# Performance work log

Hardware: AMD Instinct MI355X
Metric: run time of the kernel (lower is better)

## Reference

```python
import jax, jax.numpy as jnp
import numpy as np

EPS_NORM = 1e-6
EPS_LN = 1e-5


def setup_inputs() -> dict:
    key = jax.random.key(0)
    ks = jax.random.split(key, 6)
    b, m, d = 8, 1024, 768
    n, p = 64, 16
    h = 2 * d
    x = jax.random.normal(ks[0], (b, m, d), dtype=jnp.float32)
    phi = jax.random.normal(ks[1], (n, p, d), dtype=jnp.float32)
    # per-expert LayerNorm affine params
    ln_g = jnp.ones((n, d), dtype=jnp.float32)
    ln_b = jnp.zeros((n, d), dtype=jnp.float32)
    # per-expert MLP weights (torch Linear default init ~ U(-1/sqrt(fan_in), ...); use scaled normal)
    w1 = jax.random.normal(ks[2], (n, d, h), dtype=jnp.float32) * (1.0 / np.sqrt(d))
    b1 = jax.random.normal(ks[3], (n, h), dtype=jnp.float32) * 0.01
    w2 = jax.random.normal(ks[4], (n, h, d), dtype=jnp.float32) * (1.0 / np.sqrt(h))
    b2 = jax.random.normal(ks[5], (n, d), dtype=jnp.float32) * 0.01
    return {"x": x, "phi": phi, "ln_g": ln_g, "ln_b": ln_b,
            "w1": w1, "b1": b1, "w2": w2, "b2": b2}


def _layernorm(x, g, b):
    mu = jnp.mean(x, axis=-1, keepdims=True)
    var = jnp.mean(jnp.square(x - mu), axis=-1, keepdims=True)
    return (x - mu) * jax.lax.rsqrt(var + EPS_LN) * g + b


def reference(x, phi, ln_g, ln_b, w1, b1, w2, b2):
    # normalize phi over axis=0 (expert axis), as in the torch __init__
    phi_n = phi * jax.lax.rsqrt(jnp.sum(jnp.square(phi), axis=0, keepdims=True) + EPS_NORM)
    bsz, m, d = x.shape
    n, p, _ = phi_n.shape
    # routing logits: [b, m, n, p]
    logits = jnp.einsum('bmd,npd->bmnp', x, phi_n)
    # dispatch: softmax over tokens m
    D = jax.nn.softmax(logits, axis=1)
    # combine: softmax over flattened slots (n*p)
    C = jax.nn.softmax(logits.reshape(bsz, m, n * p), axis=-1)
    # input slots: [b, n, p, d]
    Xs = jnp.einsum('bmd,bmnp->bnpd', x, D)
    # batched per-expert MLP: LN -> Linear -> GELU -> Linear
    hdn = _layernorm(Xs, ln_g[:, None, :], ln_b[:, None, :])
    hdn = jnp.einsum('bnpd,ndh->bnph', hdn, w1) + b1[:, None, :]
    hdn = jax.nn.gelu(hdn, approximate=False)
    Ys = jnp.einsum('bnph,nhd->bnpd', hdn, w2) + b2[:, None, :]
    # combine: [b, m, d]
    Ys = Ys.reshape(bsz, n * p, d)
    Y = jnp.einsum('bsd,bms->bmd', Ys, C)
    return Y
```

## Files before the change

kernel.cpp:

```cpp
#include <hip/hip_runtime.h>
#include <math.h>

#define B 8
#define M 1024
#define D 768
#define NEXP 64
#define P 16
#define H 1536
#define S 1024
#define EPS_NORM 1e-6f
#define EPS_LN   1e-5f

typedef unsigned short u16;
typedef __attribute__((ext_vector_type(8))) short bf16x8;
typedef __attribute__((ext_vector_type(4))) float f32x4;

__device__ __forceinline__ u16 f2bf(float f) {
    union { float f; unsigned u; } v; v.f = f;
    unsigned r = v.u + 0x7FFFu + ((v.u >> 16) & 1u);
    return (u16)(r >> 16);
}

__device__ __forceinline__ float gelu_exact(float x) {
    return 0.5f * x * (1.0f + erff(x * 0.70710678118654752440f));
}

#define GLL16(g, l) __builtin_amdgcn_global_load_lds( \
    (const __attribute__((address_space(1))) void*)(g), \
    (__attribute__((address_space(3))) void*)(l), 16, 0, 0)

__device__ __forceinline__ void mfma_core_128(const u16* __restrict__ Ag,
                                              const u16* __restrict__ Bg,
                                              int K, u16* As, u16* Bs,
                                              f32x4 (&acc)[4][4]) {
    const int t    = threadIdx.x;
    const int lane = t & 63;
    const int wave = t >> 6;
    const int wr   = (wave >> 1) << 6;
    const int wc   = (wave & 1) << 6;
    const int quad = lane >> 4;
    const int l16  = lane & 15;
    const u16* ga0 = Ag + (size_t)(t >> 2) * K + (t & 3) * 8;
    const u16* ga1 = ga0 + (size_t)64 * K;
    const u16* gb0 = Bg + (size_t)(t >> 2) * K + (t & 3) * 8;
    const u16* gb1 = gb0 + (size_t)64 * K;
    u16* la0 = As + t * 8;
    u16* lb0 = Bs + t * 8;
    const u16* arp = As + (wr + l16) * 32 + quad * 8;
    const u16* brp = Bs + (wc + l16) * 32 + quad * 8;
    GLL16(ga0, la0);
    GLL16(ga1, la0 + 2048);
    GLL16(gb0, lb0);
    GLL16(gb1, lb0 + 2048);
    int cur = 0;
    for (int k0 = 0; k0 < K; k0 += 32) {
        __syncthreads();
        const int nxt = cur ^ 1;
        if (k0 + 32 < K) {
            GLL16(ga0 + k0 + 32, la0 + nxt * 4096);
            GLL16(ga1 + k0 + 32, la0 + nxt * 4096 + 2048);
            GLL16(gb0 + k0 + 32, lb0 + nxt * 4096);
            GLL16(gb1 + k0 + 32, lb0 + nxt * 4096 + 2048);
        }
        const u16* ar = arp + cur * 4096;
        const u16* br = brp + cur * 4096;
        bf16x8 af[4], bfr[4];
#pragma unroll
        for (int i = 0; i < 4; ++i) af[i]  = *(const bf16x8*)(ar + i * 512);
#pragma unroll
        for (int j = 0; j < 4; ++j) bfr[j] = *(const bf16x8*)(br + j * 512);
#pragma unroll
        for (int i = 0; i < 4; ++i)
#pragma unroll
            for (int j = 0; j < 4; ++j)
                acc[i][j] = __builtin_amdgcn_mfma_f32_16x16x32_bf16(af[i], bfr[j], acc[i][j], 0, 0, 0);
        cur = nxt;
    }
}

__device__ __forceinline__ void mfma_core_bf32(const u16* __restrict__ Ag, int K,
                                               const float* __restrict__ Bg, int ldb,
                                               u16* As, u16* Bs,
                                               f32x4 (&acc)[4][4]) {
    const int t    = threadIdx.x;
    const int lane = t & 63;
    const int wave = t >> 6;
    const int wr   = (wave >> 1) << 6;
    const int wc   = (wave & 1) << 6;
    const int quad = lane >> 4;
    const int l16  = lane & 15;
    const u16* ga0 = Ag + (size_t)(t >> 2) * K + (t & 3) * 8;
    const u16* ga1 = ga0 + (size_t)64 * K;
    u16* la0 = As + t * 8;
    const int bcol = t & 127;
    const int kq   = (t >> 7) << 4;
    const float* bg0 = Bg + (size_t)kq * ldb + bcol;
    u16* lb = Bs + bcol * 40 + kq;
    const u16* arp = As + (wr + l16) * 32 + quad * 8;
    const u16* brp = Bs + (wc + l16) * 40 + quad * 8;
    GLL16(ga0, la0);
    GLL16(ga1, la0 + 2048);
    {
        float f[16];
#pragma unroll
        for (int i = 0; i < 16; ++i) f[i] = bg0[(size_t)i * ldb];
#pragma unroll
        for (int i = 0; i < 4; ++i) {
            ushort4 o;
            o.x = f2bf(f[i*4 + 0]); o.y = f2bf(f[i*4 + 1]);
            o.z = f2bf(f[i*4 + 2]); o.w = f2bf(f[i*4 + 3]);
            *(ushort4*)(lb + i * 4) = o;
        }
    }
    int cur = 0;
    for (int k0 = 0; k0 < K; k0 += 32) {
        __syncthreads();
        const int nxt = cur ^ 1;
        const bool pf = (k0 + 32 < K);
        float f[16];
        if (pf) {
            GLL16(ga0 + k0 + 32, la0 + nxt * 4096);
            GLL16(ga1 + k0 + 32, la0 + nxt * 4096 + 2048);
            const float* bg = bg0 + (size_t)(k0 + 32) * ldb;
#pragma unroll
            for (int i = 0; i < 16; ++i) f[i] = bg[(size_t)i * ldb];
        }
        const u16* ar = arp + cur * 4096;
        const u16* br = brp + cur * 5120;
        bf16x8 af[4], bfr[4];
#pragma unroll
        for (int i = 0; i < 4; ++i) af[i]  = *(const bf16x8*)(ar + i * 512);
#pragma unroll
        for (int j = 0; j < 4; ++j) bfr[j] = *(const bf16x8*)(br + j * 640);
#pragma unroll
        for (int i = 0; i < 4; ++i)
#pragma unroll
            for (int j = 0; j < 4; ++j)
                acc[i][j] = __builtin_amdgcn_mfma_f32_16x16x32_bf16(af[i], bfr[j], acc[i][j], 0, 0, 0);
        if (pf) {
            u16* lbn = lb + nxt * 5120;
#pragma unroll
            for (int i = 0; i < 4; ++i) {
                ushort4 o;
                o.x = f2bf(f[i*4 + 0]); o.y = f2bf(f[i*4 + 1]);
                o.z = f2bf(f[i*4 + 2]); o.w = f2bf(f[i*4 + 3]);
                *(ushort4*)(lbn + i * 4) = o;
            }
        }
        cur = nxt;
    }
}

#define EPI_VARS \
    const int t = threadIdx.x; const int lane = t & 63; const int wave = t >> 6; \
    const int wr = (wave >> 1) << 6; const int wc = (wave & 1) << 6; \
    const int quad = lane >> 4; const int l16 = lane & 15; (void)t;

#define ACC_INIT \
    f32x4 acc[4][4]; \
    _Pragma("unroll") for (int i = 0; i < 4; ++i) \
    _Pragma("unroll") for (int j = 0; j < 4; ++j) acc[i][j] = (f32x4){0.f, 0.f, 0.f, 0.f};

__global__ __launch_bounds__(256) void prep_fused_kernel(const float* __restrict__ x,
                                                         const float* __restrict__ phi,
                                                         u16* __restrict__ xb,
                                                         u16* __restrict__ xT,
                                                         u16* __restrict__ phinb) {
    if (blockIdx.z == 8) {
        int bid = blockIdx.y * 12 + blockIdx.x;
        if (bid >= 48) return;
        int pos = bid * 256 + threadIdx.x;
        float ss = 0.f;
#pragma unroll 4
        for (int nn = 0; nn < NEXP; ++nn) {
            float v = phi[nn * (P*D) + pos];
            ss += v * v;
        }
        float r = rsqrtf(ss + EPS_NORM);
#pragma unroll 4
        for (int nn = 0; nn < NEXP; ++nn)
            phinb[nn * (P*D) + pos] = f2bf(phi[nn * (P*D) + pos] * r);
        return;
    }
    __shared__ float tile[64][65];
    int b = blockIdx.z;
    int m0 = blockIdx.y * 64, d0 = blockIdx.x * 64;
    int tt = threadIdx.x;
    int rr = tt >> 4, c4 = (tt & 15) * 4;
#pragma unroll
    for (int i = 0; i < 4; ++i) {
        int m = m0 + rr + i * 16;
        float4 v = *(const float4*)(x + ((size_t)b * M + m) * D + d0 + c4);
        tile[rr + i*16][c4 + 0] = v.x;
        tile[rr + i*16][c4 + 1] = v.y;
        tile[rr + i*16][c4 + 2] = v.z;
        tile[rr + i*16][c4 + 3] = v.w;
        ushort4 o;
        o.x = f2bf(v.x); o.y = f2bf(v.y); o.z = f2bf(v.z); o.w = f2bf(v.w);
        *(ushort4*)(xb + ((size_t)b * M + m) * D + d0 + c4) = o;
    }
    __syncthreads();
    int cr = tt >> 4, r4 = (tt & 15) * 4;
#pragma unroll
    for (int i = 0; i < 4; ++i) {
        int crow = cr + i * 16;
        ushort4 o;
        o.x = f2bf(tile[r4 + 0][crow]);
        o.y = f2bf(tile[r4 + 1][crow]);
        o.z = f2bf(tile[r4 + 2][crow]);
        o.w = f2bf(tile[r4 + 3][crow]);
        *(ushort4*)(xT + ((size_t)b * D + d0 + crow) * M + m0 + r4) = o;
    }
}


__global__ __launch_bounds__(256) void gemm_logits_mfma(const u16* __restrict__ xb,
                                                        const u16* __restrict__ phinb,
                                                        float* __restrict__ logits) {
    __shared__ __align__(16) u16 As[8192], Bs[8192];
    ACC_INIT;
    const int row0 = blockIdx.y * 128, col0 = blockIdx.x * 128;
    mfma_core_128(xb + (size_t)row0 * D, phinb + (size_t)col0 * D, D, As, Bs, acc);
    EPI_VARS;
#pragma unroll
    for (int i = 0; i < 4; ++i)
#pragma unroll
        for (int j = 0; j < 4; ++j) {
            int col = col0 + wc + j*16 + l16;
#pragma unroll
            for (int r = 0; r < 4; ++r) {
                int row = row0 + wr + i*16 + quad*4 + r;
                logits[(size_t)row * S + col] = acc[i][j][r];
            }
        }
}

__global__ __launch_bounds__(256) void gemm_dispatch_mfma(const u16* __restrict__ DT,
                                                          const u16* __restrict__ xT,
                                                          float* __restrict__ Xs) {
    __shared__ __align__(16) u16 As[8192], Bs[8192];
    ACC_INIT;
    const int b = blockIdx.z;
    const int row0 = blockIdx.y * 128, col0 = blockIdx.x * 128;
    mfma_core_128(DT + ((size_t)b * S + row0) * M,
                  xT + ((size_t)b * D + col0) * M, M, As, Bs, acc);
    EPI_VARS;
#pragma unroll
    for (int i = 0; i < 4; ++i)
#pragma unroll
        for (int j = 0; j < 4; ++j) {
            int col = col0 + wc + j*16 + l16;
#pragma unroll
            for (int r = 0; r < 4; ++r) {
                int row = row0 + wr + i*16 + quad*4 + r;
                Xs[((size_t)b * S + row) * D + col] = acc[i][j][r];
            }
        }
}

__global__ __launch_bounds__(256) void gemm_mlp1_mfma(const u16* __restrict__ hdnE,
                                                      const float* __restrict__ w1,
                                                      const float* __restrict__ b1,
                                                      u16* __restrict__ h1) {
    __shared__ __align__(16) u16 As[8192], Bs[10240];
    ACC_INIT;
    const int n = blockIdx.z;
    const int col0 = blockIdx.x * 128;
    mfma_core_bf32(hdnE + (size_t)n * 128 * D, D,
                   w1 + (size_t)n * D * H + col0, H, As, Bs, acc);
    EPI_VARS;
#pragma unroll
    for (int i = 0; i < 4; ++i)
#pragma unroll
        for (int j = 0; j < 4; ++j) {
            int h = col0 + wc + j*16 + l16;
            float bias = b1[n * H + h];
#pragma unroll
            for (int r = 0; r < 4; ++r) {
                int row = wr + i*16 + quad*4 + r;
                h1[((size_t)n * 128 + row) * H + h] = f2bf(gelu_exact(acc[i][j][r] + bias));
            }
        }
}

__global__ __launch_bounds__(256) void gemm_mlp2_mfma(const u16* __restrict__ h1,
                                                      const float* __restrict__ w2,
                                                      const float* __restrict__ b2,
                                                      u16* __restrict__ YsT) {
    __shared__ __align__(16) u16 As[8192], Bs[10240];
    ACC_INIT;
    const int n = blockIdx.z;
    const int col0 = blockIdx.x * 128;
    mfma_core_bf32(h1 + (size_t)n * 128 * H, H,
                   w2 + (size_t)n * H * D + col0, D, As, Bs, acc);
    EPI_VARS;
#pragma unroll
    for (int i = 0; i < 4; ++i)
#pragma unroll
        for (int j = 0; j < 4; ++j) {
            int d = col0 + wc + j*16 + l16;
            float bias = b2[n * D + d];
            int bb = ((wr + i*16) >> 4);
            int p0 = quad * 4;
            ushort4 o;
            o.x = f2bf(acc[i][j][0] + bias);
            o.y = f2bf(acc[i][j][1] + bias);
            o.z = f2bf(acc[i][j][2] + bias);
            o.w = f2bf(acc[i][j][3] + bias);
            *(ushort4*)(YsT + ((size_t)bb * D + d) * S + n * P + p0) = o;
        }
}

__global__ __launch_bounds__(256) void gemm_combine_mfma(const u16* __restrict__ Cb,
                                                         const u16* __restrict__ YsT,
                                                         float* __restrict__ out) {
    __shared__ __align__(16) u16 As[8192], Bs[8192];
    ACC_INIT;
    const int b = blockIdx.z;
    const int row0 = blockIdx.y * 128, col0 = blockIdx.x * 128;
    mfma_core_128(Cb + ((size_t)b * M + row0) * S,
                  YsT + ((size_t)b * D + col0) * S, S, As, Bs, acc);
    EPI_VARS;
#pragma unroll
    for (int i = 0; i < 4; ++i)
#pragma unroll
        for (int j = 0; j < 4; ++j) {
            int col = col0 + wc + j*16 + l16;
#pragma unroll
            for (int r = 0; r < 4; ++r) {
                int row = row0 + wr + i*16 + quad*4 + r;
                out[((size_t)b * M + row) * D + col] = acc[i][j][r];
            }
        }
}

__global__ __launch_bounds__(256) void smcol_kernel(const float* __restrict__ logits,
                                                    u16* __restrict__ Cb,
                                                    float* __restrict__ pm,
                                                    float* __restrict__ pl) {
    __shared__ float lm[3][1024], ll[3][1024];
    const int c2   = blockIdx.x;
    const int b    = c2 >> 5;
    const int mgrp = c2 & 31;
    const int t    = threadIdx.x;
    const int w    = t >> 6;
    const int lane = t & 63;
    float cm[16], cl[16];
#pragma unroll
    for (int i = 0; i < 16; ++i) { cm[i] = -INFINITY; cl[i] = 0.f; }
    const size_t rbase = (size_t)(b * 1024 + mgrp * 32 + w * 8) * 1024;
    const float* Lb = logits + rbase;
    u16* Cbb = Cb + rbase;
    for (int r = 0; r < 8; ++r) {
        const float* row = Lb + (size_t)r * 1024;
        float4 v[4];
#pragma unroll
        for (int q = 0; q < 4; ++q)
            v[q] = *(const float4*)(row + q * 256 + lane * 4);
        float mx = -INFINITY;
#pragma unroll
        for (int q = 0; q < 4; ++q)
            mx = fmaxf(mx, fmaxf(fmaxf(v[q].x, v[q].y), fmaxf(v[q].z, v[q].w)));
#pragma unroll
        for (int o = 1; o < 64; o <<= 1) mx = fmaxf(mx, __shfl_xor(mx, o));
        float4 e[4]; float sum = 0.f;
#pragma unroll
        for (int q = 0; q < 4; ++q) {
            e[q].x = expf(v[q].x - mx); e[q].y = expf(v[q].y - mx);
            e[q].z = expf(v[q].z - mx); e[q].w = expf(v[q].w - mx);
            sum += e[q].x + e[q].y + e[q].z + e[q].w;
        }
#pragma unroll
        for (int o = 1; o < 64; o <<= 1) sum += __shfl_xor(sum, o);
        float inv = 1.f / sum;
#pragma unroll
        for (int q = 0; q < 4; ++q) {
            ushort4 o4;
            o4.x = f2bf(e[q].x * inv); o4.y = f2bf(e[q].y * inv);
            o4.z = f2bf(e[q].z * inv); o4.w = f2bf(e[q].w * inv);
            *(ushort4*)(Cbb + (size_t)r * 1024 + q * 256 + lane * 4) = o4;
        }
#pragma unroll
        for (int q = 0; q < 4; ++q) {
            float vv[4] = {v[q].x, v[q].y, v[q].z, v[q].w};
#pragma unroll
            for (int j = 0; j < 4; ++j) {
                int idx = q * 4 + j;
                float nm = fmaxf(cm[idx], vv[j]);
                cl[idx] = cl[idx] * expf(cm[idx] - nm) + expf(vv[j] - nm);
                cm[idx] = nm;
            }
        }
    }
    if (w > 0) {
#pragma unroll
        for (int q = 0; q < 4; ++q)
#pragma unroll
            for (int j = 0; j < 4; ++j) {
                int col = q * 256 + lane * 4 + j;
                lm[w - 1][col] = cm[q * 4 + j];
                ll[w - 1][col] = cl[q * 4 + j];
            }
    }
    __syncthreads();
    if (w == 0) {
#pragma unroll
        for (int q = 0; q < 4; ++q)
#pragma unroll
            for (int j = 0; j < 4; ++j) {
                int idx = q * 4 + j;
                int col = q * 256 + lane * 4 + j;
#pragma unroll
                for (int wv = 0; wv < 3; ++wv) {
                    float m2 = lm[wv][col], l2 = ll[wv][col];
                    float nm = fmaxf(cm[idx], m2);
                    cl[idx] = cl[idx] * expf(cm[idx] - nm) + l2 * expf(m2 - nm);
                    cm[idx] = nm;
                }
                pm[mgrp * 8192 + b * 1024 + col] = cm[idx];
                pl[mgrp * 8192 + b * 1024 + col] = cl[idx];
            }
    }
}

__global__ __launch_bounds__(256) void dtc_kernel(const float* __restrict__ logits,
                                                  const float* __restrict__ pm,
                                                  const float* __restrict__ pl,
                                                  u16* __restrict__ DT) {
    __shared__ float tile[64][65];
    __shared__ float fmS[64], flS[64];
    const int b  = blockIdx.z;
    const int s0 = blockIdx.x * 64;
    const int m0base = blockIdx.y * 256;
    const int tt = threadIdx.x;
    if (tt < 64) {
        int col = b * 1024 + s0 + tt;
        float mx = -INFINITY;
#pragma unroll 8
        for (int c = 0; c < 32; ++c) mx = fmaxf(mx, pm[c * 8192 + col]);
        float l = 0.f;
#pragma unroll 8
        for (int c = 0; c < 32; ++c) l += pl[c * 8192 + col] * expf(pm[c * 8192 + col] - mx);
        fmS[tt] = mx;
        flS[tt] = 1.f / l;
    }
    __syncthreads();
    const int rr = tt >> 4, c4 = (tt & 15) * 4;
    const int cr = tt >> 4, r4 = (tt & 15) * 4;
    for (int sub = 0; sub < 4; ++sub) {
        const int m0 = m0base + sub * 64;
        float fm0 = fmS[c4 + 0], fm1 = fmS[c4 + 1], fm2 = fmS[c4 + 2], fm3 = fmS[c4 + 3];
        float fl0 = flS[c4 + 0], fl1 = flS[c4 + 1], fl2 = flS[c4 + 2], fl3 = flS[c4 + 3];
#pragma unroll
        for (int i = 0; i < 4; ++i) {
            float4 v = *(const float4*)(logits + ((size_t)b * M + m0 + rr + i*16) * S + s0 + c4);
            tile[rr + i*16][c4 + 0] = expf(v.x - fm0) * fl0;
            tile[rr + i*16][c4 + 1] = expf(v.y - fm1) * fl1;
            tile[rr + i*16][c4 + 2] = expf(v.z - fm2) * fl2;
            tile[rr + i*16][c4 + 3] = expf(v.w - fm3) * fl3;
        }
        __syncthreads();
#pragma unroll
        for (int i = 0; i < 4; ++i) {
            int crow = cr + i * 16;
            ushort4 o;
            o.x = f2bf(tile[r4 + 0][crow]);
            o.y = f2bf(tile[r4 + 1][crow]);
            o.z = f2bf(tile[r4 + 2][crow]);
            o.w = f2bf(tile[r4 + 3][crow]);
            *(ushort4*)(DT + ((size_t)b * S + s0 + crow) * M + m0 + r4) = o;
        }
        __syncthreads();
    }
}

__global__ __launch_bounds__(256) void layernorm_kernel(const float* __restrict__ Xs,
                                                        const float* __restrict__ g,
                                                        const float* __restrict__ bt,
                                                        u16* __restrict__ hdnE) {
    __shared__ float rs[4], rq[4];
    int row = blockIdx.x;
    int b = row >> 10;
    int n = (row >> 4) & (NEXP - 1);
    int p = row & 15;
    const float* rp = Xs + (size_t)row * D;
    u16* op = hdnE + ((size_t)n * 128 + b * 16 + p) * D;
    int t = threadIdx.x;
    float x0 = rp[t], x1 = rp[t + 256], x2 = rp[t + 512];
    float s  = x0 + x1 + x2;
    float sq = x0*x0 + x1*x1 + x2*x2;
#pragma unroll
    for (int o = 1; o < 64; o <<= 1) { s += __shfl_xor(s, o); sq += __shfl_xor(sq, o); }
    if ((t & 63) == 0) { rs[t >> 6] = s; rq[t >> 6] = sq; }
    __syncthreads();
    s  = rs[0] + rs[1] + rs[2] + rs[3];
    sq = rq[0] + rq[1] + rq[2] + rq[3];
    float mu  = s * (1.f / D);
    float var = sq * (1.f / D) - mu * mu;
    float inv = rsqrtf(var + EPS_LN);
    const float* gn = g  + n * D;
    const float* bn = bt + n * D;
    op[t]       = f2bf((x0 - mu) * inv * gn[t]       + bn[t]);
    op[t + 256] = f2bf((x1 - mu) * inv * gn[t + 256] + bn[t + 256]);
    op[t + 512] = f2bf((x2 - mu) * inv * gn[t + 512] + bn[t + 512]);
}

extern "C" void kernel_launch(void* const* d_in, const int* in_sizes, int n_in,
                              void* d_out, int out_size, void* d_ws, size_t ws_size,
                              hipStream_t stream) {
    const float* x    = (const float*)d_in[0];
    const float* phi  = (const float*)d_in[1];
    const float* ln_g = (const float*)d_in[2];
    const float* ln_b = (const float*)d_in[3];
    const float* w1   = (const float*)d_in[4];
    const float* b1   = (const float*)d_in[5];
    const float* w2   = (const float*)d_in[6];
    const float* b2   = (const float*)d_in[7];
    float* out = (float*)d_out;

    char* ws = (char*)d_ws;
    float* logits = (float*)(ws + 0);
    u16*   Cb     = (u16*)(ws + 33554432);
    u16*   xb     = (u16*)(ws + 50331648);
    u16*   DT     = (u16*)(ws + 62914560);
    u16*   xTb    = (u16*)(ws + 79691776);
    u16*   phinb  = (u16*)(ws + 92274688);
    u16*   hdnE   = (u16*)(ws + 93847552);
    float* pm     = (float*)(ws + 106430464);
    float* pl     = (float*)(ws + 107479040);
    float* Xs     = logits;
    u16*   h1     = xb;
    u16*   YsT    = xTb;

    prep_fused_kernel<<<dim3(12, 16, 9), 256, 0, stream>>>(x, phi, xb, xTb, phinb);

    gemm_logits_mfma<<<dim3(8, 64), 256, 0, stream>>>(xb, phinb, logits);
    smcol_kernel<<<256, 256, 0, stream>>>(logits, Cb, pm, pl);
    dtc_kernel<<<dim3(16, 4, B), 256, 0, stream>>>(logits, pm, pl, DT);

    gemm_dispatch_mfma<<<dim3(6, 8, B), 256, 0, stream>>>(DT, xTb, Xs);
    layernorm_kernel<<<B * S, 256, 0, stream>>>(Xs, ln_g, ln_b, hdnE);

    gemm_mlp1_mfma<<<dim3(12, 1, NEXP), 256, 0, stream>>>(hdnE, w1, b1, h1);
    gemm_mlp2_mfma<<<dim3(6, 1, NEXP), 256, 0, stream>>>(h1, w2, b2, YsT);

    gemm_combine_mfma<<<dim3(6, 8, B), 256, 0, stream>>>(Cb, YsT, out);
}
```

Baseline: 805.0 us.

## Triple-buffer LDS tiles with explicit vmcnt waits in MFMA GEMM cores

Both shared GEMM inner loops move from double-buffered LDS to a three-stage ring for the async global-to-LDS A/B tiles. Each stage waits with an explicit s_waitcnt vmcnt on only the older loads plus a raw s_barrier, instead of a full __syncthreads. This keeps two tiles in flight so global latency is hidden behind MFMA work. The cost is more LDS per block (As/Bs enlarged), which can lower occupancy, and the hand-written waitcnt counts must stay matched to the number of outstanding loads.

```diff
diff --git a/kernel.cpp b/kernel.cpp
--- a/kernel.cpp
+++ b/kernel.cpp
@@ -44,37 +44,44 @@
     const u16* ga1 = ga0 + (size_t)64 * K;
     const u16* gb0 = Bg + (size_t)(t >> 2) * K + (t & 3) * 8;
     const u16* gb1 = gb0 + (size_t)64 * K;
-    u16* la0 = As + t * 8;
-    u16* lb0 = Bs + t * 8;
-    const u16* arp = As + (wr + l16) * 32 + quad * 8;
-    const u16* brp = Bs + (wc + l16) * 32 + quad * 8;
-    GLL16(ga0, la0);
-    GLL16(ga1, la0 + 2048);
-    GLL16(gb0, lb0);
-    GLL16(gb1, lb0 + 2048);
-    int cur = 0;
+    u16 *sa0 = As + t * 8, *sa1 = sa0 + 4096, *sa2 = sa0 + 8192;
+    u16 *sb0 = Bs + t * 8, *sb1 = sb0 + 4096, *sb2 = sb0 + 8192;
+    const u16 *ra0 = As + (wr + l16) * 32 + quad * 8;
+    const u16 *ra1 = ra0 + 4096, *ra2 = ra0 + 8192;
+    const u16 *rb0 = Bs + (wc + l16) * 32 + quad * 8;
+    const u16 *rb1 = rb0 + 4096, *rb2 = rb0 + 8192;
+    GLL16(ga0, sa0); GLL16(ga1, sa0 + 2048);
+    GLL16(gb0, sb0); GLL16(gb1, sb0 + 2048);
+    if (K > 32) {
+        GLL16(ga0 + 32, sa1); GLL16(ga1 + 32, sa1 + 2048);
+        GLL16(gb0 + 32, sb1); GLL16(gb1 + 32, sb1 + 2048);
+    }
     for (int k0 = 0; k0 < K; k0 += 32) {
-        __syncthreads();
-        const int nxt = cur ^ 1;
-        if (k0 + 32 < K) {
-            GLL16(ga0 + k0 + 32, la0 + nxt * 4096);
-            GLL16(ga1 + k0 + 32, la0 + nxt * 4096 + 2048);
-            GLL16(gb0 + k0 + 32, lb0 + nxt * 4096);
-            GLL16(gb1 + k0 + 32, lb0 + nxt * 4096 + 2048);
-        }
-        const u16* ar = arp + cur * 4096;
-        const u16* br = brp + cur * 4096;
+        const int rem = ((K - k0) >> 5) - 1;
+        if (rem >= 1) asm volatile("s_waitcnt vmcnt(4)" ::: "memory");
+        else          asm volatile("s_waitcnt vmcnt(0)" ::: "memory");
+        __builtin_amdgcn_s_barrier();
+        __builtin_amdgcn_sched_barrier(0);
+        if (rem >= 2) {
+            GLL16(ga0 + k0 + 64, sa2); GLL16(ga1 + k0 + 64, sa2 + 2048);
+            GLL16(gb0 + k0 + 64, sb2); GLL16(gb1 + k0 + 64, sb2 + 2048);
+        }
         bf16x8 af[4], bfr[4];
 #pragma unroll
-        for (int i = 0; i < 4; ++i) af[i]  = *(const bf16x8*)(ar + i * 512);
-#pragma unroll
-        for (int j = 0; j < 4; ++j) bfr[j] = *(const bf16x8*)(br + j * 512);
+        for (int i = 0; i < 4; ++i) af[i]  = *(const bf16x8*)(ra0 + i * 512);
+#pragma unroll
+        for (int j = 0; j < 4; ++j) bfr[j] = *(const bf16x8*)(rb0 + j * 512);
 #pragma unroll
         for (int i = 0; i < 4; ++i)
 #pragma unroll
             for (int j = 0; j < 4; ++j)
                 acc[i][j] = __builtin_amdgcn_mfma_f32_16x16x32_bf16(af[i], bfr[j], acc[i][j], 0, 0, 0);
-        cur = nxt;
+        u16* tw;
+        tw = sa0; sa0 = sa1; sa1 = sa2; sa2 = tw;
+        tw = sb0; sb0 = sb1; sb1 = sb2; sb2 = tw;
+        const u16* tr;
+        tr = ra0; ra0 = ra1; ra1 = ra2; ra2 = tr;
+        tr = rb0; rb0 = rb1; rb1 = rb2; rb2 = tr;
     }
 }
 
@@ -91,63 +98,74 @@
     const int l16  = lane & 15;
     const u16* ga0 = Ag + (size_t)(t >> 2) * K + (t & 3) * 8;
     const u16* ga1 = ga0 + (size_t)64 * K;
-    u16* la0 = As + t * 8;
+    u16 *sa0 = As + t * 8, *sa1 = sa0 + 4096, *sa2 = sa0 + 8192;
     const int bcol = t & 127;
     const int kq   = (t >> 7) << 4;
     const float* bg0 = Bg + (size_t)kq * ldb + bcol;
-    u16* lb = Bs + bcol * 40 + kq;
-    const u16* arp = As + (wr + l16) * 32 + quad * 8;
-    const u16* brp = Bs + (wc + l16) * 40 + quad * 8;
-    GLL16(ga0, la0);
-    GLL16(ga1, la0 + 2048);
+    u16 *bw0 = Bs + bcol * 40 + kq;
+    u16 *bw1 = bw0 + 5120;
+    const u16 *rbA = Bs + (wc + l16) * 40 + quad * 8;
+    const u16 *rbB = rbA + 5120;
+    const u16 *ra0 = As + (wr + l16) * 32 + quad * 8;
+    const u16 *ra1 = ra0 + 4096, *ra2 = ra0 + 8192;
     {
         float f[16];
 #pragma unroll
         for (int i = 0; i < 16; ++i) f[i] = bg0[(size_t)i * ldb];
+        GLL16(ga0, sa0); GLL16(ga1, sa0 + 2048);
+        if (K > 32) { GLL16(ga0 + 32, sa1); GLL16(ga1 + 32, sa1 + 2048); }
 #pragma unroll
         for (int i = 0; i < 4; ++i) {
             ushort4 o;
             o.x = f2bf(f[i*4 + 0]); o.y = f2bf(f[i*4 + 1]);
             o.z = f2bf(f[i*4 + 2]); o.w = f2bf(f[i*4 + 3]);
-            *(ushort4*)(lb + i * 4) = o;
-        }
-    }
-    int cur = 0;
+            *(ushort4*)(bw0 + i * 4) = o;
+        }
+    }
+    const u16* rbc = rbA;
+    u16*       bwn = bw1;
+    const u16* rbo = rbB;
+    u16*       bwo = bw0;
     for (int k0 = 0; k0 < K; k0 += 32) {
-        __syncthreads();
-        const int nxt = cur ^ 1;
-        const bool pf = (k0 + 32 < K);
+        const int rem = ((K - k0) >> 5) - 1;
+        if (rem >= 1) asm volatile("s_waitcnt vmcnt(2) lgkmcnt(0)" ::: "memory");
+        else          asm volatile("s_waitcnt vmcnt(0) lgkmcnt(0)" ::: "memory");
+        __builtin_amdgcn_s_barrier();
+        __builtin_amdgcn_sched_barrier(0);
         float f[16];
-        if (pf) {
-            GLL16(ga0 + k0 + 32, la0 + nxt * 4096);
-            GLL16(ga1 + k0 + 32, la0 + nxt * 4096 + 2048);
+        if (rem >= 1) {
             const float* bg = bg0 + (size_t)(k0 + 32) * ldb;
 #pragma unroll
             for (int i = 0; i < 16; ++i) f[i] = bg[(size_t)i * ldb];
         }
-        const u16* ar = arp + cur * 4096;
-        const u16* br = brp + cur * 5120;
+        if (rem >= 2) {
+            GLL16(ga0 + k0 + 64, sa2); GLL16(ga1 + k0 + 64, sa2 + 2048);
+        }
         bf16x8 af[4], bfr[4];
 #pragma unroll
-        for (int i = 0; i < 4; ++i) af[i]  = *(const bf16x8*)(ar + i * 512);
-#pragma unroll
-        for (int j = 0; j < 4; ++j) bfr[j] = *(const bf16x8*)(br + j * 640);
+        for (int i = 0; i < 4; ++i) af[i]  = *(const bf16x8*)(ra0 + i * 512);
+#pragma unroll
+        for (int j = 0; j < 4; ++j) bfr[j] = *(const bf16x8*)(rbc + j * 640);
 #pragma unroll
         for (int i = 0; i < 4; ++i)
 #pragma unroll
             for (int j = 0; j < 4; ++j)
                 acc[i][j] = __builtin_amdgcn_mfma_f32_16x16x32_bf16(af[i], bfr[j], acc[i][j], 0, 0, 0);
-        if (pf) {
-            u16* lbn = lb + nxt * 5120;
+        if (rem >= 1) {
 #pragma unroll
             for (int i = 0; i < 4; ++i) {
                 ushort4 o;
                 o.x = f2bf(f[i*4 + 0]); o.y = f2bf(f[i*4 + 1]);
                 o.z = f2bf(f[i*4 + 2]); o.w = f2bf(f[i*4 + 3]);
-                *(ushort4*)(lbn + i * 4) = o;
-            }
-        }
-        cur = nxt;
+                *(ushort4*)(bwn + i * 4) = o;
+            }
+        }
+        u16* tw;
+        tw = sa0; sa0 = sa1; sa1 = sa2; sa2 = tw;
+        const u16* tr;
+        tr = ra0; ra0 = ra1; ra1 = ra2; ra2 = tr;
+        tr = rbc; rbc = rbo; rbo = tr;
+        tw = bwn; bwn = bwo; bwo = tw;
     }
 }
 
@@ -217,7 +235,7 @@
 __global__ __launch_bounds__(256) void gemm_logits_mfma(const u16* __restrict__ xb,
                                                         const u16* __restrict__ phinb,
                                                         float* __restrict__ logits) {
-    __shared__ __align__(16) u16 As[8192], Bs[8192];
+    __shared__ __align__(16) u16 As[12288], Bs[12288];
     ACC_INIT;
     const int row0 = blockIdx.y * 128, col0 = blockIdx.x * 128;
     mfma_core_128(xb + (size_t)row0 * D, phinb + (size_t)col0 * D, D, As, Bs, acc);
@@ -238,7 +256,7 @@
 __global__ __launch_bounds__(256) void gemm_dispatch_mfma(const u16* __restrict__ DT,
                                                           const u16* __restrict__ xT,
                                                           float* __restrict__ Xs) {
-    __shared__ __align__(16) u16 As[8192], Bs[8192];
+    __shared__ __align__(16) u16 As[12288], Bs[12288];
     ACC_INIT;
     const int b = blockIdx.z;
     const int row0 = blockIdx.y * 128, col0 = blockIdx.x * 128;
@@ -262,7 +280,7 @@
                                                       const float* __restrict__ w1,
                                                       const float* __restrict__ b1,
                                                       u16* __restrict__ h1) {
-    __shared__ __align__(16) u16 As[8192], Bs[10240];
+    __shared__ __align__(16) u16 As[12288], Bs[10240];
     ACC_INIT;
     const int n = blockIdx.z;
     const int col0 = blockIdx.x * 128;
@@ -287,7 +305,7 @@
                                                       const float* __restrict__ w2,
                                                       const float* __restrict__ b2,
                                                       u16* __restrict__ YsT) {
-    __shared__ __align__(16) u16 As[8192], Bs[10240];
+    __shared__ __align__(16) u16 As[12288], Bs[10240];
     ACC_INIT;
     const int n = blockIdx.z;
     const int col0 = blockIdx.x * 128;
@@ -314,7 +332,7 @@
 __global__ __launch_bounds__(256) void gemm_combine_mfma(const u16* __restrict__ Cb,
                                                          const u16* __restrict__ YsT,
                                                          float* __restrict__ out) {
-    __shared__ __align__(16) u16 As[8192], Bs[8192];
+    __shared__ __align__(16) u16 As[12288], Bs[12288];
     ACC_INIT;
     const int b = blockIdx.z;
     const int row0 = blockIdx.y * 128, col0 = blockIdx.x * 128;
```

Result: no change. 795.1 us (-1.2%).
